# Optimization experiments

Measured on AMD Instinct MI355X. Metric: run time of the kernel, lower is better.

The kernel has to match this reference:

```python
import jax, jax.numpy as jnp
import numpy as np

HIDDEN = 256
HEAD = 256
GAMMA = 0.96875
SCALE_BASE = 512  # default scale_base in the standard XPOS module


def xpos_apply(x, offset=0, downscale=False):
    """xpos rotary embedding. x: (B, S, H) with H even."""
    B, S, H = x.shape
    half = H // 2
    dt = x.dtype
    pos = jnp.arange(offset, offset + S, dtype=dt)  # (S,)
    # per-channel xpos scale: ((2i + 0.4H) / (1.4H)) ** (pos / scale_base)
    base_scale = (jnp.arange(0, H, 2, dtype=dt) + 0.4 * H) / (1.4 * H)  # (half,)
    scale = base_scale[None, :] ** (pos[:, None] / SCALE_BASE)          # (S, half)
    if downscale:
        scale = 1.0 / scale
    inv_freq = 1.0 / (10000.0 ** (jnp.arange(half, dtype=dt) / half))   # (half,)
    sinusoid = pos[:, None] * inv_freq[None, :]                         # (S, half)
    sin = jnp.sin(sinusoid) * scale
    cos = jnp.cos(sinusoid) * scale
    # duplicate-interleave columns to width H
    sin2 = jnp.repeat(sin, 2, axis=-1)  # (S, H)
    cos2 = jnp.repeat(cos, 2, axis=-1)
    # rotate_every_two
    x1 = x[..., 0::2]
    x2 = x[..., 1::2]
    rot = jnp.stack([-x2, x1], axis=-1).reshape(x.shape)
    return x * cos2[None] + rot * sin2[None]


def decay_mask(S, dtype):
    n = jnp.arange(S)
    diff = n[:, None] - n[None, :]
    # gamma^(i-j) for i>=j else 0 (clamp exponent to avoid huge values under the mask)
    D = jnp.where(diff >= 0,
                  jnp.asarray(GAMMA, dtype) ** jnp.maximum(diff, 0).astype(dtype),
                  jnp.zeros((), dtype))
    return D


def setup_inputs() -> dict:
    key = jax.random.key(0)
    k1, k2, k3, k4 = jax.random.split(key, 4)
    B, N, S = 2, 8, 2048
    X = jax.random.normal(k1, (B, N, S, HIDDEN), dtype=jnp.float32)
    # kaiming-uniform-ish init: uniform in [-1/sqrt(fan_in), 1/sqrt(fan_in)]
    bound = 1.0 / np.sqrt(HIDDEN)
    W_Q = jax.random.uniform(k2, (HIDDEN, HEAD), jnp.float32, -bound, bound)
    W_K = jax.random.uniform(k3, (HIDDEN, HEAD), jnp.float32, -bound, bound)
    W_V = jax.random.uniform(k4, (HIDDEN, HEAD), jnp.float32, -bound, bound)
    return {"X": X, "W_Q": W_Q, "W_K": W_K, "W_V": W_V}


def reference(X, W_Q, W_K, W_V):
    B, N, S, H = X.shape
    Q = X @ W_Q  # (B, N, S, head)
    K = X @ W_K
    V = X @ W_V
    hd = Q.shape[-1]
    Q = xpos_apply(Q.reshape(B * N, S, hd)).reshape(B, N, S, hd)
    K = xpos_apply(K.reshape(B * N, S, hd), downscale=True).reshape(B, N, S, hd)
    D = decay_mask(S, X.dtype)  # (S, S)
    scores = jnp.einsum('bnsh,bnth->bnst', Q, K) * D  # (B, N, S, S)
    return scores @ V  # (B, N, S, v_dim)
```

## Files before the change

### kernel.cpp

```cpp
#include <hip/hip_runtime.h>
#include <hip/hip_bf16.h>


#define S_LEN 2048
#define HD 256
#define BN 16

typedef _Float16 half8 __attribute__((ext_vector_type(8)));
typedef _Float16 half4 __attribute__((ext_vector_type(4)));
typedef _Float16 half2v __attribute__((ext_vector_type(2)));
typedef float floatx16 __attribute__((ext_vector_type(16)));

__device__ __forceinline__ void gl_lds16(const void* g, void* l) {
  __builtin_amdgcn_global_load_lds(
      (const __attribute__((address_space(1))) unsigned int*)(unsigned long long)g,
      (__attribute__((address_space(3))) unsigned int*)(unsigned int)(unsigned long long)l,
      16, 0, 0);
}

__global__ __launch_bounds__(256) void prep_kernel(
    const float* __restrict__ WQ, const float* __restrict__ WK,
    const float* __restrict__ WV, _Float16* __restrict__ WT,
    _Float16* __restrict__ TBL) {
  const int b = blockIdx.x;
  const int tid = threadIdx.x;
  if (b < 1024) {
    const int idx = b * 256 + tid;
    const int i2 = idx & 127;
    const int pos = idx >> 7;
    float inv_freq = exp2f(-(float)i2 * (13.287712379549449f / 128.0f));
    float lbase = log2f(((float)(2 * i2) + 102.4f) / 358.4f);
    float ang = (float)pos * inv_freq;
    float sn, cs;
    sincosf(ang, &sn, &cs);
    float scl = exp2f((float)pos * (1.0f / 512.0f) * lbase);
    float rscl = 1.0f / scl;
    half2v tq, tk;
    tq[0] = (_Float16)(cs * scl);  tq[1] = (_Float16)(sn * scl);
    tk[0] = (_Float16)(cs * rscl); tk[1] = (_Float16)(sn * rscl);
    *(half2v*)&TBL[(long)idx * 2] = tq;
    *(half2v*)&TBL[(long)(262144 + idx) * 2] = tk;
    return;
  }
  __shared__ _Float16 trans[64][72];
  const int bb = b - 1024;
  const int w = bb >> 4;
  const int tk = ((bb & 15) & 3) * 64;
  const int tn = ((bb & 15) >> 2) * 64;
  const float* W = (w == 0) ? WQ : (w == 1) ? WK : WV;
#pragma unroll
  for (int u = 0; u < 4; ++u) {
    int idx = u * 256 + tid;
    int k = idx >> 4;
    int nq = (idx & 15) * 4;
    float4 v = *(const float4*)&W[(tk + k) * HD + tn + nq];
    trans[nq + 0][k] = (_Float16)v.x;
    trans[nq + 1][k] = (_Float16)v.y;
    trans[nq + 2][k] = (_Float16)v.z;
    trans[nq + 3][k] = (_Float16)v.w;
  }
  __syncthreads();
#pragma unroll
  for (int u = 0; u < 2; ++u) {
    int idx = u * 256 + tid;
    int n = idx >> 3;
    int kq = (idx & 7) * 8;
    *(uint4*)&WT[((long)w * HD + tn + n) * HD + tk + kq] = *(const uint4*)&trans[n][kq];
  }
}

__global__ __launch_bounds__(256) void gemm_qkv_kernel(
    const float* __restrict__ X, const _Float16* __restrict__ WT,
    const _Float16* __restrict__ TBL,
    _Float16* __restrict__ Q, _Float16* __restrict__ K,
    _Float16* __restrict__ VT) {
  __shared__ __align__(16) unsigned char smem[66560];
  unsigned char* ep = smem + 32768;

  const int tid = threadIdx.x;
  const int lane = tid & 63;
  const int w = tid >> 6;
  const int l31 = lane & 31;
  const int lh = lane >> 5;
  const int m0 = blockIdx.x * 64;

#pragma unroll
  for (int i = 0; i < 8; ++i) {
    int id = i * 256 + tid;
    int row = id >> 5, c = id & 31;
    int p = c ^ (row & 31);
    const float4* s = (const float4*)&X[(long)(m0 + row) * HD + c * 8];
    float4 v0 = s[0], v1 = s[1];
    half8 h;
    h[0] = (_Float16)v0.x; h[1] = (_Float16)v0.y;
    h[2] = (_Float16)v0.z; h[3] = (_Float16)v0.w;
    h[4] = (_Float16)v1.x; h[5] = (_Float16)v1.y;
    h[6] = (_Float16)v1.z; h[7] = (_Float16)v1.w;
    *(half8*)(smem + row * 512 + p * 16) = h;
  }
  __syncthreads();

  const int bn = m0 >> 11;
  const int srow0 = m0 & (S_LEN - 1);
  const int ncol0 = w * 64;

  for (int wsel = 0; wsel < 3; ++wsel) {
    const _Float16* Wb = WT + (long)wsel * HD * HD;
    floatx16 acc[2][2];
#pragma unroll
    for (int mt = 0; mt < 2; ++mt)
#pragma unroll
      for (int nt = 0; nt < 2; ++nt)
#pragma unroll
        for (int e = 0; e < 16; ++e) acc[mt][nt][e] = 0.f;

    half8 b[5][2];
#pragma unroll
    for (int pk = 0; pk < 5; ++pk)
#pragma unroll
      for (int nt = 0; nt < 2; ++nt)
        b[pk][nt] = *(const half8*)(Wb + (long)(ncol0 + nt * 32 + l31) * HD +
                                    pk * 16 + lh * 8);
#pragma unroll
    for (int ks16 = 0; ks16 < 16; ++ks16) {
      const int slot = ks16 % 5;
      int p = (ks16 * 2 + lh) ^ l31;
      half8 af0 = *(const half8*)(smem + l31 * 512 + p * 16);
      half8 af1 = *(const half8*)(smem + (32 + l31) * 512 + p * 16);
#pragma unroll
      for (int nt = 0; nt < 2; ++nt) {
        acc[0][nt] = __builtin_amdgcn_mfma_f32_32x32x16_f16(af0, b[slot][nt], acc[0][nt], 0, 0, 0);
        acc[1][nt] = __builtin_amdgcn_mfma_f32_32x32x16_f16(af1, b[slot][nt], acc[1][nt], 0, 0, 0);
      }
      if (ks16 + 5 < 16) {
#pragma unroll
        for (int nt = 0; nt < 2; ++nt)
          b[slot][nt] = *(const half8*)(Wb + (long)(ncol0 + nt * 32 + l31) * HD +
                                        (ks16 + 5) * 16 + lh * 8);
      }
    }

    if (wsel < 2) {
#pragma unroll
      for (int mt = 0; mt < 2; ++mt)
#pragma unroll
        for (int nt = 0; nt < 2; ++nt) {
          int col = ncol0 + nt * 32 + l31;
#pragma unroll
          for (int reg = 0; reg < 16; ++reg) {
            int rmap = (reg & 3) + 8 * (reg >> 2) + 4 * lh;
            *(_Float16*)(ep + (mt * 32 + rmap) * 528 + col * 2) =
                (_Float16)acc[mt][nt][reg];
          }
        }
      __syncthreads();
      _Float16* o = wsel ? K : Q;
      const _Float16* tb_base = TBL + (long)wsel * 2048 * 128 * 2;
#pragma unroll
      for (int u = 0; u < 8; ++u) {
        int id = u * 256 + tid;
        int row = id >> 5;
        int cq = (id & 31) * 8;
        half8 x = *(const half8*)(ep + row * 528 + cq * 2);
        half8 t = *(const half8*)&tb_base[((long)(srow0 + row) * 128 + (cq >> 1)) * 2];
        half8 y;
        y[0] = x[0] * t[0] - x[1] * t[1];
        y[1] = x[1] * t[0] + x[0] * t[1];
        y[2] = x[2] * t[2] - x[3] * t[3];
        y[3] = x[3] * t[2] + x[2] * t[3];
        y[4] = x[4] * t[4] - x[5] * t[5];
        y[5] = x[5] * t[4] + x[4] * t[5];
        y[6] = x[6] * t[6] - x[7] * t[7];
        y[7] = x[7] * t[6] + x[6] * t[7];
        *(half8*)&o[(long)(m0 + row) * HD + cq] = y;
      }
      __syncthreads();
    } else {
      __syncthreads();
      _Float16 (*vt)[72] = (_Float16(*)[72])smem;
#pragma unroll
      for (int mt = 0; mt < 2; ++mt)
#pragma unroll
        for (int nt = 0; nt < 2; ++nt) {
          int h = ncol0 + nt * 32 + l31;
#pragma unroll
          for (int reg = 0; reg < 16; ++reg) {
            int rmap = (reg & 3) + 8 * (reg >> 2) + 4 * lh;
            vt[h][mt * 32 + rmap] = (_Float16)acc[mt][nt][reg];
          }
        }
      __syncthreads();
#pragma unroll
      for (int u = 0; u < 8; ++u) {
        int id = u * 256 + tid;
        int h = id >> 3, sj = (id & 7) * 8;
        *(uint4*)&VT[((long)bn * HD + h) * S_LEN + srow0 + sj] = *(const uint4*)&vt[h][sj];
      }
    }
  }
}

__global__ __launch_bounds__(256) void retention_kernel(
    const _Float16* __restrict__ Q, const _Float16* __restrict__ K,
    const _Float16* __restrict__ VT, float* __restrict__ out) {
  __shared__ __align__(16) unsigned char smem[74752];
  unsigned char* ksb = smem;
  unsigned char* vsb = smem + 32768;
  _Float16 (*sc)[72] = (_Float16(*)[72])(smem + 65536);

  const int tid = threadIdx.x;
  const int lane = tid & 63;
  const int w = tid >> 6;
  const int l31 = lane & 31;
  const int lh = lane >> 5;
  const int qtile = w >> 1;
  const int ttile = w & 1;
  const int hhalf = w & 1;

  const int L = blockIdx.x;
  const int head = L & 15;
  const int g4 = L >> 4;
  const int qt = (g4 < 16) ? (31 - g4) : (g4 - 16);
  const int q0 = qt * 64;

  const _Float16* Qh = Q + (long)head * S_LEN * HD;
  const _Float16* Kh = K + (long)head * S_LEN * HD;
  const _Float16* VTh = VT + (long)head * HD * S_LEN;

  half8 qf[16];
  {
    const _Float16* qrow = Qh + (long)(q0 + qtile * 32 + l31) * HD + lh * 8;
#pragma unroll
    for (int ks16 = 0; ks16 < 16; ++ks16)
      qf[ks16] = *(const half8*)(qrow + ks16 * 16);
  }

  floatx16 acc[4];
#pragma unroll
  for (int nt = 0; nt < 4; ++nt)
#pragma unroll
    for (int e = 0; e < 16; ++e) acc[nt][e] = 0.f;

  const float LG = -0.0458036896f;
  float Cg[16];
#pragma unroll
  for (int g = 0; g < 4; ++g)
#pragma unroll
    for (int r = 0; r < 4; ++r) Cg[4 * g + r] = exp2f(-(float)(8 * g + r) * LG);

#define STAGE_K(T0)                                                        \
  {                                                                        \
    _Pragma("unroll") for (int j = 0; j < 8; ++j) {                        \
      int li = w * 8 + j;                                                  \
      int row = li * 2 + lh;                                               \
      int c = l31 ^ (row & 31);                                            \
      gl_lds16(Kh + (long)((T0) + row) * HD + c * 8, ksb + li * 1024);     \
    }                                                                      \
  }
#define STAGE_V(T0)                                                        \
  {                                                                        \
    _Pragma("unroll") for (int j = 0; j < 8; ++j) {                        \
      int li = w * 8 + j;                                                  \
      int row = li * 8 + (lane >> 3);                                      \
      int c = (lane & 7) ^ (row & 7);                                      \
      gl_lds16(VTh + (long)row * S_LEN + (T0) + c * 8, vsb + li * 1024);   \
    }                                                                      \
  }

  STAGE_K(0);
  STAGE_V(0);

  for (int kt = 0; kt <= qt; ++kt) {
    const int t0 = kt * 64;
    asm volatile("s_waitcnt vmcnt(0)" ::: "memory");
    __syncthreads();

    floatx16 s;
#pragma unroll
    for (int e = 0; e < 16; ++e) s[e] = 0.f;
    {
      const unsigned char* kbase = ksb + (ttile * 32 + l31) * 512;
#pragma unroll
      for (int ks16 = 0; ks16 < 16; ++ks16) {
        int p = (ks16 * 2 + lh) ^ l31;
        half8 a = *(const half8*)(kbase + p * 16);
        s = __builtin_amdgcn_mfma_f32_32x32x16_f16(a, qf[ks16], s, 0, 0, 0);
      }
    }

    {
      const int qg = q0 + qtile * 32 + l31;
      const int tb = t0 + ttile * 32 + 4 * lh;
      const int dd = qg - tb;
      const float E = exp2f((float)dd * LG);
#pragma unroll
      for (int g = 0; g < 4; ++g) {
        half4 h4;
#pragma unroll
        for (int r = 0; r < 4; ++r) {
          int o = 8 * g + r;
          float wv = (dd >= o) ? E * Cg[4 * g + r] : 0.f;
          h4[r] = (_Float16)(s[4 * g + r] * wv);
        }
        *(half4*)&sc[qtile * 32 + l31][ttile * 32 + 4 * lh + 8 * g] = h4;
      }
    }
    __syncthreads();

    if (kt < qt) STAGE_K(t0 + 64);

#pragma unroll
    for (int kst = 0; kst < 4; ++kst) {
      half8 a = *(const half8*)&sc[qtile * 32 + l31][kst * 16 + lh * 8];
#pragma unroll
      for (int nt = 0; nt < 4; ++nt) {
        int h = hhalf * 128 + nt * 32 + l31;
        int p = (kst * 2 + lh) ^ (h & 7);
        half8 b = *(const half8*)(vsb + h * 128 + p * 16);
        acc[nt] = __builtin_amdgcn_mfma_f32_32x32x16_f16(a, b, acc[nt], 0, 0, 0);
      }
    }
    asm volatile("s_waitcnt vmcnt(0)" ::: "memory");
    __syncthreads();

    if (kt < qt) STAGE_V(t0 + 64);
  }

  const long rbase = (long)head * S_LEN + q0 + qtile * 32;
#pragma unroll
  for (int nt = 0; nt < 4; ++nt) {
    int col = hhalf * 128 + nt * 32 + l31;
#pragma unroll
    for (int reg = 0; reg < 16; ++reg) {
      int rmap = (reg & 3) + 8 * (reg >> 2) + 4 * lh;
      out[(rbase + rmap) * HD + col] = acc[nt][reg];
    }
  }
}

extern "C" void kernel_launch(void* const* d_in, const int* in_sizes, int n_in,
                              void* d_out, int out_size, void* d_ws, size_t ws_size,
                              hipStream_t stream) {
  const float* X  = (const float*)d_in[0];
  const float* WQ = (const float*)d_in[1];
  const float* WK = (const float*)d_in[2];
  const float* WV = (const float*)d_in[3];
  float* out = (float*)d_out;

  _Float16* Qh = (_Float16*)d_ws;
  _Float16* Kh = Qh + (size_t)BN * S_LEN * HD;
  _Float16* VTh = Kh + (size_t)BN * S_LEN * HD;
  _Float16* WT = VTh + (size_t)BN * S_LEN * HD;
  _Float16* TBL = WT + (size_t)3 * HD * HD;

  prep_kernel<<<dim3(1072), dim3(256), 0, stream>>>(WQ, WK, WV, WT, TBL);
  gemm_qkv_kernel<<<dim3((BN * S_LEN) / 64), dim3(256), 0, stream>>>(
      X, WT, TBL, Qh, Kh, VTh);
  retention_kernel<<<dim3(512), dim3(256), 0, stream>>>(Qh, Kh, VTh, out);
}
```

Measured before the change: 174.5 us.

## Use 512-thread blocks in QKV GEMM with one 32-column tile per wave

```diff
diff --git a/kernel.cpp b/kernel.cpp
--- a/kernel.cpp
+++ b/kernel.cpp
@@ -69,7 +69,7 @@
   }
 }
 
-__global__ __launch_bounds__(256) void gemm_qkv_kernel(
+__global__ __launch_bounds__(512) void gemm_qkv_kernel(
     const float* __restrict__ X, const _Float16* __restrict__ WT,
     const _Float16* __restrict__ TBL,
     _Float16* __restrict__ Q, _Float16* __restrict__ K,
@@ -85,8 +85,8 @@
   const int m0 = blockIdx.x * 64;
 
 #pragma unroll
-  for (int i = 0; i < 8; ++i) {
-    int id = i * 256 + tid;
+  for (int i = 0; i < 4; ++i) {
+    int id = i * 512 + tid;
     int row = id >> 5, c = id & 31;
     int p = c ^ (row & 31);
     const float4* s = (const float4*)&X[(long)(m0 + row) * HD + c * 8];
@@ -102,63 +102,49 @@
 
   const int bn = m0 >> 11;
   const int srow0 = m0 & (S_LEN - 1);
-  const int ncol0 = w * 64;
+  const int ncol0 = w * 32;
 
   for (int wsel = 0; wsel < 3; ++wsel) {
     const _Float16* Wb = WT + (long)wsel * HD * HD;
-    floatx16 acc[2][2];
+    floatx16 acc[2];
 #pragma unroll
     for (int mt = 0; mt < 2; ++mt)
 #pragma unroll
-      for (int nt = 0; nt < 2; ++nt)
-#pragma unroll
-        for (int e = 0; e < 16; ++e) acc[mt][nt][e] = 0.f;
-
-    half8 b[5][2];
+      for (int e = 0; e < 16; ++e) acc[mt][e] = 0.f;
+
+    half8 b[5];
 #pragma unroll
     for (int pk = 0; pk < 5; ++pk)
-#pragma unroll
-      for (int nt = 0; nt < 2; ++nt)
-        b[pk][nt] = *(const half8*)(Wb + (long)(ncol0 + nt * 32 + l31) * HD +
-                                    pk * 16 + lh * 8);
+      b[pk] = *(const half8*)(Wb + (long)(ncol0 + l31) * HD + pk * 16 + lh * 8);
 #pragma unroll
     for (int ks16 = 0; ks16 < 16; ++ks16) {
       const int slot = ks16 % 5;
       int p = (ks16 * 2 + lh) ^ l31;
       half8 af0 = *(const half8*)(smem + l31 * 512 + p * 16);
       half8 af1 = *(const half8*)(smem + (32 + l31) * 512 + p * 16);
-#pragma unroll
-      for (int nt = 0; nt < 2; ++nt) {
-        acc[0][nt] = __builtin_amdgcn_mfma_f32_32x32x16_f16(af0, b[slot][nt], acc[0][nt], 0, 0, 0);
-        acc[1][nt] = __builtin_amdgcn_mfma_f32_32x32x16_f16(af1, b[slot][nt], acc[1][nt], 0, 0, 0);
-      }
-      if (ks16 + 5 < 16) {
-#pragma unroll
-        for (int nt = 0; nt < 2; ++nt)
-          b[slot][nt] = *(const half8*)(Wb + (long)(ncol0 + nt * 32 + l31) * HD +
-                                        (ks16 + 5) * 16 + lh * 8);
-      }
+      acc[0] = __builtin_amdgcn_mfma_f32_32x32x16_f16(af0, b[slot], acc[0], 0, 0, 0);
+      acc[1] = __builtin_amdgcn_mfma_f32_32x32x16_f16(af1, b[slot], acc[1], 0, 0, 0);
+      if (ks16 + 5 < 16)
+        b[slot] = *(const half8*)(Wb + (long)(ncol0 + l31) * HD +
+                                  (ks16 + 5) * 16 + lh * 8);
     }
 
     if (wsel < 2) {
+      const int col = ncol0 + l31;
 #pragma unroll
       for (int mt = 0; mt < 2; ++mt)
 #pragma unroll
-        for (int nt = 0; nt < 2; ++nt) {
-          int col = ncol0 + nt * 32 + l31;
-#pragma unroll
-          for (int reg = 0; reg < 16; ++reg) {
-            int rmap = (reg & 3) + 8 * (reg >> 2) + 4 * lh;
-            *(_Float16*)(ep + (mt * 32 + rmap) * 528 + col * 2) =
-                (_Float16)acc[mt][nt][reg];
-          }
+        for (int reg = 0; reg < 16; ++reg) {
+          int rmap = (reg & 3) + 8 * (reg >> 2) + 4 * lh;
+          *(_Float16*)(ep + (mt * 32 + rmap) * 528 + col * 2) =
+              (_Float16)acc[mt][reg];
         }
       __syncthreads();
       _Float16* o = wsel ? K : Q;
       const _Float16* tb_base = TBL + (long)wsel * 2048 * 128 * 2;
 #pragma unroll
-      for (int u = 0; u < 8; ++u) {
-        int id = u * 256 + tid;
+      for (int u = 0; u < 4; ++u) {
+        int id = u * 512 + tid;
         int row = id >> 5;
         int cq = (id & 31) * 8;
         half8 x = *(const half8*)(ep + row * 528 + cq * 2);
@@ -178,23 +164,20 @@
     } else {
       __syncthreads();
       _Float16 (*vt)[72] = (_Float16(*)[72])smem;
+      const int h = ncol0 + l31;
 #pragma unroll
       for (int mt = 0; mt < 2; ++mt)
 #pragma unroll
-        for (int nt = 0; nt < 2; ++nt) {
-          int h = ncol0 + nt * 32 + l31;
-#pragma unroll
-          for (int reg = 0; reg < 16; ++reg) {
-            int rmap = (reg & 3) + 8 * (reg >> 2) + 4 * lh;
-            vt[h][mt * 32 + rmap] = (_Float16)acc[mt][nt][reg];
-          }
+        for (int reg = 0; reg < 16; ++reg) {
+          int rmap = (reg & 3) + 8 * (reg >> 2) + 4 * lh;
+          vt[h][mt * 32 + rmap] = (_Float16)acc[mt][reg];
         }
       __syncthreads();
 #pragma unroll
-      for (int u = 0; u < 8; ++u) {
-        int id = u * 256 + tid;
-        int h = id >> 3, sj = (id & 7) * 8;
-        *(uint4*)&VT[((long)bn * HD + h) * S_LEN + srow0 + sj] = *(const uint4*)&vt[h][sj];
+      for (int u = 0; u < 4; ++u) {
+        int id = u * 512 + tid;
+        int hh = id >> 3, sj = (id & 7) * 8;
+        *(uint4*)&VT[((long)bn * HD + hh) * S_LEN + srow0 + sj] = *(const uint4*)&vt[hh][sj];
       }
     }
   }
@@ -354,7 +337,7 @@
   _Float16* TBL = WT + (size_t)3 * HD * HD;
 
   prep_kernel<<<dim3(1072), dim3(256), 0, stream>>>(WQ, WK, WV, WT, TBL);
-  gemm_qkv_kernel<<<dim3((BN * S_LEN) / 64), dim3(256), 0, stream>>>(
+  gemm_qkv_kernel<<<dim3((BN * S_LEN) / 64), dim3(512), 0, stream>>>(
       X, WT, TBL, Qh, Kh, VTh);
   retention_kernel<<<dim3(512), dim3(256), 0, stream>>>(Qh, Kh, VTh, out);
 }
```

Result: no change. 173.4 us (-0.6%).
